# Performance work log

Measured on AMD Instinct MI355X. Metric: run time of the kernel, lower is better.

## Reference

```python
import jax, jax.numpy as jnp
import numpy as np

N_NODES = 100000
N_EDGES = 1600000
D_IN, D_HID, D_OUT = 32, 16, 2


def graph_conv(x, edge_index, w_rel, w_root, b):
    # PyG GraphConv (aggr='add'): out_i = x_i @ W_root^T + (sum_{j in N(i)} x_j) @ W_rel^T + b
    src, dst = edge_index[0], edge_index[1]
    msgs = x[src]                                            # [E, d] neighbor gather
    agg = jax.ops.segment_sum(msgs, dst, num_segments=N_NODES)  # [N, d] scatter-add
    return agg @ w_rel.T + x @ w_root.T + b


def setup_inputs() -> dict:
    key = jax.random.key(0)
    ks = jax.random.split(key, 8)
    x = jax.random.normal(ks[0], (N_NODES, D_IN), dtype=jnp.float32)
    edge_index = jax.random.randint(ks[1], (2, N_EDGES), 0, N_NODES, dtype=jnp.int64)
    def glorot(k, shape):
        lim = np.sqrt(6.0 / (shape[0] + shape[1]))
        return jax.random.uniform(k, shape, jnp.float32, -lim, lim)
    w1_rel = glorot(ks[2], (D_HID, D_IN))
    w1_root = glorot(ks[3], (D_HID, D_IN))
    b1 = jnp.zeros((D_HID,), jnp.float32)
    w2_rel = glorot(ks[4], (D_OUT, D_HID))
    w2_root = glorot(ks[5], (D_OUT, D_HID))
    b2 = jnp.zeros((D_OUT,), jnp.float32)
    return {"x": x, "edge_index": edge_index,
            "w1_rel": w1_rel, "w1_root": w1_root, "b1": b1,
            "w2_rel": w2_rel, "w2_root": w2_root, "b2": b2}


def reference(x, edge_index, w1_rel, w1_root, b1, w2_rel, w2_root, b2):
    h = graph_conv(x, edge_index, w1_rel, w1_root, b1)
    h = jax.nn.relu(h)
    out = graph_conv(h, edge_index, w2_rel, w2_root, b2)
    return out
```

## Files before the change

### kernel.cpp

```cpp
#include <hip/hip_runtime.h>

#define N_NODES 100000
#define N_EDGES 1600000
#define D_IN 32
#define D_HID 16
#define D_OUT 2

#define NPB 128
#define NB 782
#define NROWS (NB * NPB)
#define CHUNK 4096
#define BBLOCKS ((N_EDGES + CHUNK - 1) / CHUNK)

#define PBC 2560
#define DUMMY_SRC 100000u
#define DUMMY_REC ((127u << 17) | DUMMY_SRC)
#define PAD_ALIGN 16

#define ACC2_K 16
#define ACC2_BPB 2
#define ACC2_BLOCKS (NB * ACC2_BPB)


__device__ __forceinline__ unsigned bfr(float x) {
    unsigned u = __float_as_uint(x);
    return (u + 0x7FFFu + ((u >> 16) & 1u)) >> 16;
}
__device__ __forceinline__ float bfu(unsigned lo16) {
    return __uint_as_float(lo16 << 16);
}

__global__ __launch_bounds__(512) void k_bin_node1(
    const int* __restrict__ ei, const float* __restrict__ x,
    const float* __restrict__ w_rel, const float* __restrict__ w_root,
    const float* __restrict__ bb,
    unsigned short* __restrict__ xr, float* __restrict__ agg,
    int* __restrict__ gcur, unsigned* __restrict__ recs2)
{
    __shared__ int cnt[NB];
    __shared__ int lcnt[NB];
    __shared__ int loff[NB];
    __shared__ int gbase[NB];
    __shared__ unsigned sorted[CHUNK];
    __shared__ unsigned short bkt16[CHUNK];
    __shared__ float s_rel[D_HID * D_IN];
    __shared__ float s_root[D_HID * D_IN];
    __shared__ float s_b[D_HID];
    int blk = blockIdx.x, tid = threadIdx.x;

    for (int i = tid; i < D_HID * D_IN; i += 512) {
        s_rel[i]  = w_rel[i];
        s_root[i] = w_root[i];
    }
    if (tid < D_HID) s_b[tid] = bb[tid];
    for (int i = tid; i < NB; i += 512) { cnt[i] = 0; lcnt[i] = 0; }
    __syncthreads();

    int e0 = blk * CHUNK;
    int e1 = min(e0 + CHUNK, N_EDGES);
    for (int e = e0 + tid; e < e1; e += 512)
        atomicAdd(&cnt[ei[N_EDGES + e] >> 7], 1);

    int node = blk * 512 + tid;
    if (node == N_NODES) {
        uint4* xp = (uint4*)(xr + (size_t)node * D_HID);
        xp[0] = make_uint4(0, 0, 0, 0);
        xp[1] = make_uint4(0, 0, 0, 0);
    } else if (node < N_NODES) {
        float row[D_IN];
        const float4* xp = (const float4*)(x + (size_t)node * D_IN);
#pragma unroll
        for (int i = 0; i < D_IN / 4; i++) {
            float4 v = xp[i];
            row[4*i+0] = v.x; row[4*i+1] = v.y; row[4*i+2] = v.z; row[4*i+3] = v.w;
        }
        float oa[D_HID], orr[D_HID];
#pragma unroll
        for (int o = 0; o < D_HID; o++) {
            float a = 0.f, r = s_b[o];
#pragma unroll
            for (int k = 0; k < D_IN; k++) {
                a += row[k] * s_rel[o * D_IN + k];
                r += row[k] * s_root[o * D_IN + k];
            }
            oa[o] = a; orr[o] = r;
        }
        unsigned p[8];
#pragma unroll
        for (int i = 0; i < 8; i++)
            p[i] = bfr(oa[2*i]) | (bfr(oa[2*i+1]) << 16);
        uint4* xrp = (uint4*)(xr + (size_t)node * D_HID);
        xrp[0] = make_uint4(p[0], p[1], p[2], p[3]);
        xrp[1] = make_uint4(p[4], p[5], p[6], p[7]);
        float4* aggp = (float4*)(agg + (size_t)node * D_HID);
#pragma unroll
        for (int i = 0; i < D_HID / 4; i++)
            aggp[i] = make_float4(orr[4*i], orr[4*i+1], orr[4*i+2], orr[4*i+3]);
    }
    __syncthreads();

    if (tid < 64) {
        int running = 0;
        for (int c = 0; c < (NB + 63) / 64; c++) {
            int idx = c * 64 + tid;
            int v = (idx < NB) ? cnt[idx] : 0;
            int incl = v;
#pragma unroll
            for (int off = 1; off < 64; off <<= 1) {
                int t = __shfl_up(incl, off);
                if (tid >= off) incl += t;
            }
            if (idx < NB) loff[idx] = running + incl - v;
            running += __shfl(incl, 63);
        }
    } else {
        for (int i = tid - 64; i < NB; i += 448)
            gbase[i] = (cnt[i] > 0) ? atomicAdd(&gcur[i], cnt[i]) : 0;
    }
    __syncthreads();

    for (int e = e0 + tid; e < e1; e += 512) {
        int src = ei[e];
        int dst = ei[N_EDGES + e];
        int bkt = dst >> 7;
        int r = atomicAdd(&lcnt[bkt], 1);
        int p = loff[bkt] + r;
        sorted[p] = ((unsigned)(dst & (NPB - 1)) << 17) | (unsigned)src;
        bkt16[p] = (unsigned short)bkt;
    }
    __syncthreads();

    int n4 = e1 - e0;
    for (int i = tid; i < n4; i += 512) {
        int b = bkt16[i];
        int idx = gbase[b] + (i - loff[b]);
        if (idx < PBC)
            recs2[b * PBC + idx] = sorted[i];
    }
}

__global__ __launch_bounds__(512) void k_sortacc(
    const int* __restrict__ gcur, unsigned* __restrict__ recs2,
    const unsigned short* __restrict__ srcf, float* __restrict__ dstf,
    const float* __restrict__ w_rel2, const float* __restrict__ w_root2,
    const float* __restrict__ bb2,
    float* __restrict__ hr, float* __restrict__ outv)
{
    __shared__ unsigned stage[PBC];
    __shared__ unsigned sorted[PBC];
    __shared__ int hist[NPB], sc[NPB], cur[NPB];
    __shared__ float s_rel2[D_OUT * D_HID];
    __shared__ float s_root2[D_OUT * D_HID];
    __shared__ float s_b2[D_OUT];
    int b = blockIdx.x, tid = threadIdx.x;
    int n = min(gcur[b], PBC);
    unsigned* w = recs2 + (size_t)b * PBC;

    if (tid < D_OUT * D_HID) {
        s_rel2[tid]  = w_rel2[tid];
        s_root2[tid] = w_root2[tid];
    }
    if (tid < D_OUT) s_b2[tid] = bb2[tid];

    if (tid < NPB) hist[tid] = 0;
    for (int i = tid; i < n; i += 512) stage[i] = w[i];
    __syncthreads();
    for (int i = tid; i < n; i += 512)
        atomicAdd(&hist[stage[i] >> 17], 1);
    __syncthreads();
    if (tid < NPB) sc[tid] = hist[tid];
    __syncthreads();
#pragma unroll
    for (int off = 1; off < NPB; off <<= 1) {
        int t = (tid >= off && tid < NPB) ? sc[tid - off] : 0;
        __syncthreads();
        if (tid < NPB) sc[tid] += t;
        __syncthreads();
    }
    if (tid < NPB) cur[tid] = sc[tid] - hist[tid];
    __syncthreads();
    for (int i = tid; i < n; i += 512) {
        unsigned r = stage[i];
        int slot = atomicAdd(&cur[r >> 17], 1);
        sorted[slot] = r;
    }
    int npad = (n + PAD_ALIGN - 1) & ~(PAD_ALIGN - 1);
    for (int i = n + tid; i < npad; i += 512) sorted[i] = DUMMY_REC;
    __syncthreads();

    for (int i = tid; i < npad; i += 512) w[i] = sorted[i];

    int g = tid >> 4;
    int f = tid & (D_HID - 1);
    int dbase = b * NPB;
    for (int base = g * 16; base < npad; base += 32 * 16) {
        unsigned e[16];
#pragma unroll
        for (int k = 0; k < 16; k++) e[k] = sorted[base + k];
        float v[16];
#pragma unroll
        for (int k = 0; k < 16; k++)
            v[k] = bfu(srcf[(e[k] & 0x1FFFF) * D_HID + f]);

        unsigned curd = e[0] >> 17;
        float acc = v[0];
#pragma unroll
        for (int k = 1; k < 16; k++) {
            unsigned dl = e[k] >> 17;
            if (dl == curd) {
                acc += v[k];
            } else {
                atomicAdd(&dstf[(dbase + curd) * D_HID + f], acc);
                curd = dl;
                acc = v[k];
            }
        }
        atomicAdd(&dstf[(dbase + curd) * D_HID + f], acc);
    }

    __syncthreads();
    if (tid < NPB) {
        int node = dbase + tid;
        if (node < N_NODES) {
            float h[D_HID];
            const float4* ap = (const float4*)(dstf + (size_t)node * D_HID);
#pragma unroll
            for (int i = 0; i < D_HID / 4; i++) {
                float4 vv = ap[i];
                h[4*i+0] = fmaxf(vv.x, 0.f); h[4*i+1] = fmaxf(vv.y, 0.f);
                h[4*i+2] = fmaxf(vv.z, 0.f); h[4*i+3] = fmaxf(vv.w, 0.f);
            }
            float o_rel[D_OUT], o_root[D_OUT];
#pragma unroll
            for (int o = 0; o < D_OUT; o++) {
                float a = 0.f, r = s_b2[o];
#pragma unroll
                for (int k = 0; k < D_HID; k++) {
                    a += h[k] * s_rel2[o * D_HID + k];
                    r += h[k] * s_root2[o * D_HID + k];
                }
                o_rel[o] = a; o_root[o] = r;
            }
            ((float2*)hr)[node]   = make_float2(o_rel[0], o_rel[1]);
            ((float2*)outv)[node] = make_float2(o_root[0], o_root[1]);
        } else if (node == N_NODES) {
            ((float2*)hr)[node] = make_float2(0.f, 0.f);
        }
    }
}

__global__ __launch_bounds__(256) void k_acc2(
    const unsigned* __restrict__ recs2, const int* __restrict__ gcur,
    const float* __restrict__ hr, float* __restrict__ outv)
{
    int bucket = blockIdx.x / ACC2_BPB;
    int blk    = blockIdx.x % ACC2_BPB;
    int g = threadIdx.x >> 1;
    int f = threadIdx.x & 1;
    int r0 = (blk * 128 + g) * ACC2_K;
    int n = min(gcur[bucket], PBC);
    if (r0 >= n) return;
    const unsigned* rp = recs2 + (size_t)bucket * PBC + r0;

    unsigned e[ACC2_K];
#pragma unroll
    for (int k = 0; k < ACC2_K; k++) e[k] = rp[k];
    float v[ACC2_K];
#pragma unroll
    for (int k = 0; k < ACC2_K; k++)
        v[k] = hr[(e[k] & 0x1FFFF) * D_OUT + f];

    int dbase = bucket * NPB;
    unsigned cur = e[0] >> 17;
    float acc = v[0];
#pragma unroll
    for (int k = 1; k < ACC2_K; k++) {
        unsigned dl = e[k] >> 17;
        if (dl == cur) {
            acc += v[k];
        } else {
            int d = dbase + (int)cur;
            if (d < N_NODES) atomicAdd(&outv[d * D_OUT + f], acc);
            cur = dl;
            acc = v[k];
        }
    }
    int d = dbase + (int)cur;
    if (d < N_NODES) atomicAdd(&outv[d * D_OUT + f], acc);
}

extern "C" void kernel_launch(void* const* d_in, const int* in_sizes, int n_in,
                              void* d_out, int out_size, void* d_ws, size_t ws_size,
                              hipStream_t stream) {
    const float* x       = (const float*)d_in[0];
    const int*   ei      = (const int*)  d_in[1];
    const float* w1_rel  = (const float*)d_in[2];
    const float* w1_root = (const float*)d_in[3];
    const float* b1      = (const float*)d_in[4];
    const float* w2_rel  = (const float*)d_in[5];
    const float* w2_root = (const float*)d_in[6];
    const float* b2      = (const float*)d_in[7];
    float* out = (float*)d_out;

    float*          agg   = (float*)d_ws;
    unsigned short* xrh   = (unsigned short*)(agg + (size_t)NROWS * D_HID);
    unsigned*       recs2 = (unsigned*)(xrh + (size_t)NROWS * D_HID);
    float*          hr    = (float*)(recs2 + (size_t)NB * PBC);
    int*            gcur  = (int*)(hr + (size_t)NROWS * D_OUT);

    hipMemsetAsync(gcur, 0, NB * sizeof(int), stream);

    k_bin_node1<<<dim3(BBLOCKS), dim3(512), 0, stream>>>(
        ei, x, w1_rel, w1_root, b1, xrh, agg, gcur, recs2);

    k_sortacc<<<dim3(NB), dim3(512), 0, stream>>>(
        gcur, recs2, xrh, agg, w2_rel, w2_root, b2, hr, out);

    k_acc2<<<dim3(ACC2_BLOCKS), dim3(256), 0, stream>>>(recs2, gcur, hr, out);
}
```

Measured before the change: 160.9 us.

## Replace block-local counting sort with direct per-edge global atomics for binning

After: 509.0 us. 3.16x slower.

```diff
diff --git a/kernel.cpp b/kernel.cpp
--- a/kernel.cpp
+++ b/kernel.cpp
@@ -11,6 +11,7 @@
 #define NROWS (NB * NPB)
 #define CHUNK 4096
 #define BBLOCKS ((N_EDGES + CHUNK - 1) / CHUNK)
+#define EPT 8
 
 #define PBC 2560
 #define DUMMY_SRC 100000u
@@ -37,12 +38,6 @@
     unsigned short* __restrict__ xr, float* __restrict__ agg,
     int* __restrict__ gcur, unsigned* __restrict__ recs2)
 {
-    __shared__ int cnt[NB];
-    __shared__ int lcnt[NB];
-    __shared__ int loff[NB];
-    __shared__ int gbase[NB];
-    __shared__ unsigned sorted[CHUNK];
-    __shared__ unsigned short bkt16[CHUNK];
     __shared__ float s_rel[D_HID * D_IN];
     __shared__ float s_root[D_HID * D_IN];
     __shared__ float s_b[D_HID];
@@ -53,13 +48,18 @@
         s_root[i] = w_root[i];
     }
     if (tid < D_HID) s_b[tid] = bb[tid];
-    for (int i = tid; i < NB; i += 512) { cnt[i] = 0; lcnt[i] = 0; }
-    __syncthreads();
 
     int e0 = blk * CHUNK;
     int e1 = min(e0 + CHUNK, N_EDGES);
-    for (int e = e0 + tid; e < e1; e += 512)
-        atomicAdd(&cnt[ei[N_EDGES + e] >> 7], 1);
+    int srcs[EPT], dsts[EPT];
+#pragma unroll
+    for (int k = 0; k < EPT; k++) {
+        int e = e0 + tid + k * 512;
+        bool ok = e < e1;
+        srcs[k] = ok ? ei[e] : 0;
+        dsts[k] = ok ? ei[N_EDGES + e] : -1;
+    }
+    __syncthreads();
 
     int node = blk * 512 + tid;
     if (node == N_NODES) {
@@ -97,45 +97,17 @@
         for (int i = 0; i < D_HID / 4; i++)
             aggp[i] = make_float4(orr[4*i], orr[4*i+1], orr[4*i+2], orr[4*i+3]);
     }
-    __syncthreads();
-
-    if (tid < 64) {
-        int running = 0;
-        for (int c = 0; c < (NB + 63) / 64; c++) {
-            int idx = c * 64 + tid;
-            int v = (idx < NB) ? cnt[idx] : 0;
-            int incl = v;
-#pragma unroll
-            for (int off = 1; off < 64; off <<= 1) {
-                int t = __shfl_up(incl, off);
-                if (tid >= off) incl += t;
-            }
-            if (idx < NB) loff[idx] = running + incl - v;
-            running += __shfl(incl, 63);
-        }
-    } else {
-        for (int i = tid - 64; i < NB; i += 448)
-            gbase[i] = (cnt[i] > 0) ? atomicAdd(&gcur[i], cnt[i]) : 0;
-    }
-    __syncthreads();
-
-    for (int e = e0 + tid; e < e1; e += 512) {
-        int src = ei[e];
-        int dst = ei[N_EDGES + e];
-        int bkt = dst >> 7;
-        int r = atomicAdd(&lcnt[bkt], 1);
-        int p = loff[bkt] + r;
-        sorted[p] = ((unsigned)(dst & (NPB - 1)) << 17) | (unsigned)src;
-        bkt16[p] = (unsigned short)bkt;
-    }
-    __syncthreads();
-
-    int n4 = e1 - e0;
-    for (int i = tid; i < n4; i += 512) {
-        int b = bkt16[i];
-        int idx = gbase[b] + (i - loff[b]);
-        if (idx < PBC)
-            recs2[b * PBC + idx] = sorted[i];
+
+    int idx[EPT];
+#pragma unroll
+    for (int k = 0; k < EPT; k++)
+        idx[k] = (dsts[k] >= 0) ? atomicAdd(&gcur[dsts[k] >> 7], 1) : PBC;
+#pragma unroll
+    for (int k = 0; k < EPT; k++) {
+        if (idx[k] < PBC) {
+            unsigned rec = ((unsigned)(dsts[k] & (NPB - 1)) << 17) | (unsigned)srcs[k];
+            recs2[(size_t)(dsts[k] >> 7) * PBC + idx[k]] = rec;
+        }
     }
 }
 
```

## Cache edges in registers and reuse histogram atomic ranks in counting sorts

Applied to the files above, without the earlier changes.

Result: faster. 152.0 us (-5.5%).

```diff
diff --git a/kernel.cpp b/kernel.cpp
--- a/kernel.cpp
+++ b/kernel.cpp
@@ -9,8 +9,9 @@
 #define NPB 128
 #define NB 782
 #define NROWS (NB * NPB)
-#define CHUNK 4096
-#define BBLOCKS ((N_EDGES + CHUNK - 1) / CHUNK)
+#define CHUNK 6400
+#define BBLOCKS 250
+#define EPT 13
 
 #define PBC 2560
 #define DUMMY_SRC 100000u
@@ -38,7 +39,6 @@
     int* __restrict__ gcur, unsigned* __restrict__ recs2)
 {
     __shared__ int cnt[NB];
-    __shared__ int lcnt[NB];
     __shared__ int loff[NB];
     __shared__ int gbase[NB];
     __shared__ unsigned sorted[CHUNK];
@@ -47,19 +47,30 @@
     __shared__ float s_root[D_HID * D_IN];
     __shared__ float s_b[D_HID];
     int blk = blockIdx.x, tid = threadIdx.x;
+    int e0 = blk * CHUNK;
+
+    int srcs[EPT], dsts[EPT];
+#pragma unroll
+    for (int k = 0; k < EPT; k++) {
+        int off = tid + k * 512;
+        bool ok = off < CHUNK;
+        int e = e0 + off;
+        srcs[k] = ok ? ei[e] : 0;
+        dsts[k] = ok ? ei[N_EDGES + e] : -1;
+    }
 
     for (int i = tid; i < D_HID * D_IN; i += 512) {
         s_rel[i]  = w_rel[i];
         s_root[i] = w_root[i];
     }
     if (tid < D_HID) s_b[tid] = bb[tid];
-    for (int i = tid; i < NB; i += 512) { cnt[i] = 0; lcnt[i] = 0; }
-    __syncthreads();
-
-    int e0 = blk * CHUNK;
-    int e1 = min(e0 + CHUNK, N_EDGES);
-    for (int e = e0 + tid; e < e1; e += 512)
-        atomicAdd(&cnt[ei[N_EDGES + e] >> 7], 1);
+    for (int i = tid; i < NB; i += 512) cnt[i] = 0;
+    __syncthreads();
+
+    int rank[EPT];
+#pragma unroll
+    for (int k = 0; k < EPT; k++)
+        rank[k] = (dsts[k] >= 0) ? atomicAdd(&cnt[dsts[k] >> 7], 1) : 0;
 
     int node = blk * 512 + tid;
     if (node == N_NODES) {
@@ -119,19 +130,18 @@
     }
     __syncthreads();
 
-    for (int e = e0 + tid; e < e1; e += 512) {
-        int src = ei[e];
-        int dst = ei[N_EDGES + e];
-        int bkt = dst >> 7;
-        int r = atomicAdd(&lcnt[bkt], 1);
-        int p = loff[bkt] + r;
-        sorted[p] = ((unsigned)(dst & (NPB - 1)) << 17) | (unsigned)src;
-        bkt16[p] = (unsigned short)bkt;
-    }
-    __syncthreads();
-
-    int n4 = e1 - e0;
-    for (int i = tid; i < n4; i += 512) {
+#pragma unroll
+    for (int k = 0; k < EPT; k++) {
+        if (dsts[k] >= 0) {
+            int bkt = dsts[k] >> 7;
+            int p = loff[bkt] + rank[k];
+            sorted[p] = ((unsigned)(dsts[k] & (NPB - 1)) << 17) | (unsigned)srcs[k];
+            bkt16[p] = (unsigned short)bkt;
+        }
+    }
+    __syncthreads();
+
+    for (int i = tid; i < CHUNK; i += 512) {
         int b = bkt16[i];
         int idx = gbase[b] + (i - loff[b]);
         if (idx < PBC)
@@ -148,7 +158,7 @@
 {
     __shared__ unsigned stage[PBC];
     __shared__ unsigned sorted[PBC];
-    __shared__ int hist[NPB], sc[NPB], cur[NPB];
+    __shared__ int hist[NPB], base[NPB];
     __shared__ float s_rel2[D_OUT * D_HID];
     __shared__ float s_root2[D_OUT * D_HID];
     __shared__ float s_b2[D_OUT];
@@ -165,24 +175,40 @@
     if (tid < NPB) hist[tid] = 0;
     for (int i = tid; i < n; i += 512) stage[i] = w[i];
     __syncthreads();
-    for (int i = tid; i < n; i += 512)
-        atomicAdd(&hist[stage[i] >> 17], 1);
-    __syncthreads();
-    if (tid < NPB) sc[tid] = hist[tid];
-    __syncthreads();
-#pragma unroll
-    for (int off = 1; off < NPB; off <<= 1) {
-        int t = (tid >= off && tid < NPB) ? sc[tid - off] : 0;
-        __syncthreads();
-        if (tid < NPB) sc[tid] += t;
-        __syncthreads();
-    }
-    if (tid < NPB) cur[tid] = sc[tid] - hist[tid];
-    __syncthreads();
-    for (int i = tid; i < n; i += 512) {
-        unsigned r = stage[i];
-        int slot = atomicAdd(&cur[r >> 17], 1);
-        sorted[slot] = r;
+
+    unsigned rc[PBC / 512];
+    int rk[PBC / 512];
+#pragma unroll
+    for (int j = 0; j < PBC / 512; j++) {
+        int i = tid + j * 512;
+        if (i < n) {
+            rc[j] = stage[i];
+            rk[j] = atomicAdd(&hist[rc[j] >> 17], 1);
+        } else {
+            rc[j] = DUMMY_REC; rk[j] = -1;
+        }
+    }
+    __syncthreads();
+
+    if (tid < 64) {
+        int v0 = hist[tid], v1 = hist[tid + 64];
+        int s0 = v0, s1 = v1;
+#pragma unroll
+        for (int off = 1; off < 64; off <<= 1) {
+            int t0 = __shfl_up(s0, off);
+            int t1 = __shfl_up(s1, off);
+            if (tid >= off) { s0 += t0; s1 += t1; }
+        }
+        int tot0 = __shfl(s0, 63);
+        base[tid]      = s0 - v0;
+        base[tid + 64] = tot0 + s1 - v1;
+    }
+    __syncthreads();
+
+#pragma unroll
+    for (int j = 0; j < PBC / 512; j++) {
+        if (rk[j] >= 0)
+            sorted[base[rc[j] >> 17] + rk[j]] = rc[j];
     }
     int npad = (n + PAD_ALIGN - 1) & ~(PAD_ALIGN - 1);
     for (int i = n + tid; i < npad; i += 512) sorted[i] = DUMMY_REC;
@@ -193,10 +219,10 @@
     int g = tid >> 4;
     int f = tid & (D_HID - 1);
     int dbase = b * NPB;
-    for (int base = g * 16; base < npad; base += 32 * 16) {
+    for (int bse = g * 16; bse < npad; bse += 32 * 16) {
         unsigned e[16];
 #pragma unroll
-        for (int k = 0; k < 16; k++) e[k] = sorted[base + k];
+        for (int k = 0; k < 16; k++) e[k] = sorted[bse + k];
         float v[16];
 #pragma unroll
         for (int k = 0; k < 16; k++)
```
